# Optimization experiments

Measured on AMD Instinct MI355X. Metric: run time of the kernel, lower is better.

Reference implementation:

```python
import jax, jax.numpy as jnp
import numpy as np

B, T, D = 4, 2048, 768
D_CONV, D_GRIF, D_FFN, K = 384, 384, 2048, 3
EPS = 1e-6


def rmsnorm(x, w):
    rms = jax.lax.rsqrt(jnp.mean(jnp.square(x.astype(jnp.float32)), axis=-1, keepdims=True) + EPS)
    return (x.astype(jnp.float32) * rms).astype(x.dtype) * w


def causal_dwconv(x, w):
    # x: [B,T,C], w: [C,K] depthwise causal conv
    k = w.shape[1]
    xp = jnp.pad(x, ((0, 0), (k - 1, 0), (0, 0)))  # left pad -> causal
    out = jax.lax.conv_general_dilated(
        xp.transpose(0, 2, 1), w[:, None, :],  # [B,C,T+K-1], [C,1,K]
        window_strides=(1,), padding='VALID',
        dimension_numbers=('NCW', 'OIW', 'NCW'),
        feature_group_count=w.shape[0])
    return out.transpose(0, 2, 1)  # [B,T,C]


def rg_lru(v, r, i, lam):
    # Griffin RG-LRU: log_a = -8*softplus(lam)*r; h_t = a*h_{t-1} + sqrt(1-a^2)*(i*v)
    log_a = -8.0 * jax.nn.softplus(lam) * r                # [B,T,Dg]
    a = jnp.exp(log_a)
    gated = jnp.sqrt(jnp.maximum(1.0 - jnp.exp(2.0 * log_a), EPS)) * (i * v)
    def comb(c1, c2):
        a1, b1 = c1
        a2, b2 = c2
        return (a1 * a2, a2 * b1 + b2)
    _, h = jax.lax.associative_scan(comb, (a, gated), axis=1)
    return h


def setup_inputs() -> dict:
    key = jax.random.key(0)
    ks = jax.random.split(key, 16)
    s_in = 1.0 / np.sqrt(D)
    s_ffn = 1.0 / np.sqrt(D_FFN)
    return {
        'x': jax.random.normal(ks[0], (B, T, D), jnp.float32),
        'velocity': jnp.zeros((B, T, D), jnp.float32),
        'pre_norm_w': jnp.ones((D,), jnp.float32),
        'conv_in_w': jax.random.normal(ks[1], (D, 2 * D_CONV), jnp.float32) * s_in,
        'conv_dw_w': jax.random.normal(ks[2], (D_CONV, K), jnp.float32) * (1.0 / np.sqrt(K)),
        'grif_v_w': jax.random.normal(ks[3], (D, D_GRIF), jnp.float32) * s_in,
        'grif_r_w': jax.random.normal(ks[4], (D, D_GRIF), jnp.float32) * s_in,
        'grif_i_w': jax.random.normal(ks[5], (D, D_GRIF), jnp.float32) * s_in,
        'grif_lam': jax.random.uniform(ks[6], (D_GRIF,), jnp.float32, 0.5, 2.0),
        'out_w': jax.random.normal(ks[7], (D, D), jnp.float32) * s_in,
        'log_beta': jnp.array(0.0, jnp.float32),  # log(0.5/(1-0.5))
        'ffn_norm_w': jnp.ones((D,), jnp.float32),
        'w1': jax.random.normal(ks[8], (D, D_FFN), jnp.float32) * s_in,
        'w3': jax.random.normal(ks[9], (D, D_FFN), jnp.float32) * s_in,
        'w2': jax.random.normal(ks[10], (D_FFN, D), jnp.float32) * s_ffn,
    }


def reference(x, velocity, pre_norm_w, conv_in_w, conv_dw_w, grif_v_w, grif_r_w,
              grif_i_w, grif_lam, out_w, log_beta, ffn_norm_w, w1, w3, w2):
    xn = rmsnorm(x, pre_norm_w)
    # GatedConv branch -> [B,T,D_CONV]
    u, g = jnp.split(xn @ conv_in_w, 2, axis=-1)
    conv_out = causal_dwconv(u, conv_dw_w) * jax.nn.silu(g)
    # Griffin RG-LRU branch -> [B,T,D_GRIF]
    v = xn @ grif_v_w
    r = jax.nn.sigmoid(xn @ grif_r_w)
    i = jax.nn.sigmoid(xn @ grif_i_w)
    griffin_out = rg_lru(v, r, i, grif_lam)
    # concat -> out_proj -> momentum residual
    mixer_out = jnp.concatenate([conv_out, griffin_out], axis=-1) @ out_w
    beta = jax.nn.sigmoid(log_beta)
    velocity = beta * velocity + mixer_out
    x = x + velocity
    # ffn: RMSNorm -> SwiGLU -> residual
    normed = rmsnorm(x, ffn_norm_w)
    x = x + (jax.nn.silu(normed @ w1) * (normed @ w3)) @ w2
    return (x, velocity)
```

## Files before the change

kernel.cpp:

```cpp
#include <hip/hip_runtime.h>
#include <hip/hip_bf16.h>
#include <cstdint>

#define BSZ   4
#define TSEQ  2048
#define DMOD  768
#define DCONV 384
#define DGRIF 384
#define DFFN  2048
#define BT    (BSZ*TSEQ)
#define NG1   1920
#define EPS_  1e-6f

typedef __bf16 bf16;
typedef __bf16 bf16x8 __attribute__((ext_vector_type(8)));
typedef float  f32x4  __attribute__((ext_vector_type(4)));

__device__ __forceinline__ float sigmoidf_(float x) { return 1.f / (1.f + __expf(-x)); }

__device__ __forceinline__ void gload_lds16(const void* g, void* l) {
  __builtin_amdgcn_global_load_lds(
      (const __attribute__((address_space(1))) void*)(uintptr_t)g,
      (__attribute__((address_space(3))) void*)(uint32_t)(uintptr_t)l,
      16, 0, 0);
}

__device__ __forceinline__ int swz_wg() {
  const int nwg = gridDim.x;
  const int bid = blockIdx.x;
  const int cpx = nwg >> 3;
  return (bid & 7) * cpx + (bid >> 3);
}


template <int MODE>
__global__ __launch_bounds__(256) void transpose_bf16_kernel(
    const float* __restrict__ W, bf16* __restrict__ Wt, int R, int C, int half)
{
  __shared__ float tile[32][33];
  const int tc = blockIdx.x * 32;
  const int tr = blockIdx.y * 32;
  const int lx = threadIdx.x;
  const int ly = threadIdx.y;
  #pragma unroll
  for (int i = ly; i < 32; i += 8) {
    int r = tr + i, c = tc + lx;
    tile[i][lx] = (r < R && c < C) ? W[(size_t)r * C + c] : 0.f;
  }
  __syncthreads();
  #pragma unroll
  for (int i = ly; i < 32; i += 8) {
    int oc = tc + i;
    int orr = tr + lx;
    if (oc < C && orr < R) {
      int orow = (MODE == 0) ? oc : ((oc >> 6) << 7) + half + (oc & 63);
      Wt[(size_t)orow * R + orr] = (bf16)tile[lx][i];
    }
  }
}

__global__ __launch_bounds__(256) void rmsnorm_kernel(
    const float* __restrict__ x, const float* __restrict__ w, bf16* __restrict__ out)
{
  __shared__ float sbuf[4];
  const int row = blockIdx.x;
  const int tid = threadIdx.x;
  const float* xr = x + (size_t)row * DMOD;
  float v0 = xr[tid], v1 = xr[tid + 256], v2 = xr[tid + 512];
  float s = v0*v0 + v1*v1 + v2*v2;
  #pragma unroll
  for (int o = 32; o > 0; o >>= 1) s += __shfl_down(s, o, 64);
  if ((tid & 63) == 0) sbuf[tid >> 6] = s;
  __syncthreads();
  float tot = sbuf[0] + sbuf[1] + sbuf[2] + sbuf[3];
  float rms = rsqrtf(tot * (1.f / (float)DMOD) + EPS_);
  bf16* orow = out + (size_t)row * DMOD;
  orow[tid]       = (bf16)(v0 * rms * w[tid]);
  orow[tid + 256] = (bf16)(v1 * rms * w[tid + 256]);
  orow[tid + 512] = (bf16)(v2 * rms * w[tid + 512]);
}

__global__ __launch_bounds__(256) void gemm_w128(
    const bf16* __restrict__ A, const bf16* __restrict__ Bt, bf16* __restrict__ C,
    int M, int N, int K, int nx)
{
  __shared__ alignas(16) unsigned short As[128 * 64];
  __shared__ alignas(16) unsigned short Bs[128 * 64];

  const int wg = swz_wg();
  const int m0 = (wg / nx) * 128, n0 = (wg % nx) * 128;
  const int tid  = threadIdx.x;
  const int wave = tid >> 6;
  const int lane = tid & 63;
  const int wr = wave >> 1, wc = wave & 1;

  f32x4 acc[4][4] = {};
  const int srow = lane >> 3;
  const int scol = ((lane & 7) ^ srow) * 8;
  const int lr = lane & 15;
  const int lsw = lr & 7;
  const int lk4 = lane >> 4;

  for (int k0 = 0; k0 < K; k0 += 64) {
    __syncthreads();
    #pragma unroll
    for (int it = 0; it < 4; ++it) {
      const int chunk = wave * 4 + it;
      const int row = chunk * 8 + srow;
      gload_lds16(A  + (size_t)(m0 + row) * K + k0 + scol, (char*)As + chunk * 1024);
      gload_lds16(Bt + (size_t)(n0 + row) * K + k0 + scol, (char*)Bs + chunk * 1024);
    }
    __syncthreads();
    #pragma unroll
    for (int kk = 0; kk < 2; ++kk) {
      bf16x8 af[4], bfr[4];
      #pragma unroll
      for (int i = 0; i < 4; ++i)
        af[i] = *reinterpret_cast<const bf16x8*>(
            &As[(wr*64 + i*16 + lr) * 64 + (((kk*4 + lk4) ^ lsw) * 8)]);
      #pragma unroll
      for (int i = 0; i < 4; ++i)
        bfr[i] = *reinterpret_cast<const bf16x8*>(
            &Bs[(wc*64 + i*16 + lr) * 64 + (((kk*4 + lk4) ^ lsw) * 8)]);
      #pragma unroll
      for (int mi = 0; mi < 4; ++mi)
        #pragma unroll
        for (int ni = 0; ni < 4; ++ni)
          acc[mi][ni] = __builtin_amdgcn_mfma_f32_16x16x32_bf16(af[mi], bfr[ni], acc[mi][ni], 0, 0, 0);
    }
  }

  #pragma unroll
  for (int mi = 0; mi < 4; ++mi)
    #pragma unroll
    for (int ni = 0; ni < 4; ++ni)
      #pragma unroll
      for (int reg = 0; reg < 4; ++reg) {
        const int r = m0 + wr*64 + mi*16 + (lane >> 4) * 4 + reg;
        const int c = n0 + wc*64 + ni*16 + (lane & 15);
        C[(size_t)r * N + c] = (bf16)acc[mi][ni][reg];
      }
}

__global__ __launch_bounds__(256) void gemm_ffn13(
    const bf16* __restrict__ A, const bf16* __restrict__ Bt, bf16* __restrict__ H,
    int M, int K, int nx)
{
  __shared__ alignas(16) unsigned short As[128 * 64];
  __shared__ alignas(16) unsigned short Bs[128 * 64];
  bf16* comb = reinterpret_cast<bf16*>(As);

  const int wg = swz_wg();
  const int m0 = (wg / nx) * 128;
  const int bx = wg % nx;
  const int n0 = bx * 128;
  const int tid  = threadIdx.x;
  const int wave = tid >> 6;
  const int lane = tid & 63;
  const int wr = wave >> 1, wc = wave & 1;

  f32x4 acc[4][4] = {};
  const int srow = lane >> 3;
  const int scol = ((lane & 7) ^ srow) * 8;
  const int lr = lane & 15;
  const int lsw = lr & 7;
  const int lk4 = lane >> 4;

  for (int k0 = 0; k0 < K; k0 += 64) {
    __syncthreads();
    #pragma unroll
    for (int it = 0; it < 4; ++it) {
      const int chunk = wave * 4 + it;
      const int row = chunk * 8 + srow;
      gload_lds16(A  + (size_t)(m0 + row) * K + k0 + scol, (char*)As + chunk * 1024);
      gload_lds16(Bt + (size_t)(n0 + row) * K + k0 + scol, (char*)Bs + chunk * 1024);
    }
    __syncthreads();
    #pragma unroll
    for (int kk = 0; kk < 2; ++kk) {
      bf16x8 af[4], bfr[4];
      #pragma unroll
      for (int i = 0; i < 4; ++i)
        af[i] = *reinterpret_cast<const bf16x8*>(
            &As[(wr*64 + i*16 + lr) * 64 + (((kk*4 + lk4) ^ lsw) * 8)]);
      #pragma unroll
      for (int i = 0; i < 4; ++i)
        bfr[i] = *reinterpret_cast<const bf16x8*>(
            &Bs[(wc*64 + i*16 + lr) * 64 + (((kk*4 + lk4) ^ lsw) * 8)]);
      #pragma unroll
      for (int mi = 0; mi < 4; ++mi)
        #pragma unroll
        for (int ni = 0; ni < 4; ++ni)
          acc[mi][ni] = __builtin_amdgcn_mfma_f32_16x16x32_bf16(af[mi], bfr[ni], acc[mi][ni], 0, 0, 0);
    }
  }

  __syncthreads();
  if (wc == 1) {
    #pragma unroll
    for (int mi = 0; mi < 4; ++mi)
      #pragma unroll
      for (int ni = 0; ni < 4; ++ni)
        #pragma unroll
        for (int reg = 0; reg < 4; ++reg) {
          const int row = wr*64 + mi*16 + (lane >> 4) * 4 + reg;
          const int col = ni*16 + (lane & 15);
          comb[row * 64 + col] = (bf16)acc[mi][ni][reg];
        }
  }
  __syncthreads();
  if (wc == 0) {
    #pragma unroll
    for (int mi = 0; mi < 4; ++mi)
      #pragma unroll
      for (int ni = 0; ni < 4; ++ni)
        #pragma unroll
        for (int reg = 0; reg < 4; ++reg) {
          const int row = wr*64 + mi*16 + (lane >> 4) * 4 + reg;
          const int col = ni*16 + (lane & 15);
          float p3 = (float)comb[row * 64 + col];
          float p1 = acc[mi][ni][reg];
          H[(size_t)(m0 + row) * DFFN + bx * 64 + col] = (bf16)(p1 * sigmoidf_(p1) * p3);
        }
  }
}

template <int EPI>
__global__ __launch_bounds__(256) void gemm_n64(
    const bf16* __restrict__ A, const bf16* __restrict__ Bt, float* __restrict__ C,
    const float* __restrict__ xin, const float* __restrict__ vin,
    float* __restrict__ outv, const float* __restrict__ log_beta,
    int M, int N, int K, int nx)
{
  __shared__ alignas(16) unsigned short As[128 * 64];
  __shared__ alignas(16) unsigned short Bs[64 * 64];

  const int wg = swz_wg();
  const int m0 = (wg / nx) * 128, n0 = (wg % nx) * 64;
  const int tid  = threadIdx.x;
  const int wave = tid >> 6;
  const int lane = tid & 63;
  const int wr = wave >> 1, wc = wave & 1;

  f32x4 acc[4][2] = {};
  const int srow = lane >> 3;
  const int scol = ((lane & 7) ^ srow) * 8;
  const int lr = lane & 15;
  const int lsw = lr & 7;
  const int lk4 = lane >> 4;

  for (int k0 = 0; k0 < K; k0 += 64) {
    __syncthreads();
    #pragma unroll
    for (int it = 0; it < 6; ++it) {
      const int chunk = wave * 6 + it;
      if (chunk < 16) {
        const int row = chunk * 8 + srow;
        gload_lds16(A + (size_t)(m0 + row) * K + k0 + scol, (char*)As + chunk * 1024);
      } else {
        const int row = (chunk - 16) * 8 + srow;
        gload_lds16(Bt + (size_t)(n0 + row) * K + k0 + scol, (char*)Bs + (chunk - 16) * 1024);
      }
    }
    __syncthreads();
    #pragma unroll
    for (int kk = 0; kk < 2; ++kk) {
      bf16x8 af[4], bfr[2];
      #pragma unroll
      for (int i = 0; i < 4; ++i)
        af[i] = *reinterpret_cast<const bf16x8*>(
            &As[(wr*64 + i*16 + lr) * 64 + (((kk*4 + lk4) ^ lsw) * 8)]);
      #pragma unroll
      for (int i = 0; i < 2; ++i)
        bfr[i] = *reinterpret_cast<const bf16x8*>(
            &Bs[(wc*32 + i*16 + lr) * 64 + (((kk*4 + lk4) ^ lsw) * 8)]);
      #pragma unroll
      for (int mi = 0; mi < 4; ++mi)
        #pragma unroll
        for (int ni = 0; ni < 2; ++ni)
          acc[mi][ni] = __builtin_amdgcn_mfma_f32_16x16x32_bf16(af[mi], bfr[ni], acc[mi][ni], 0, 0, 0);
    }
  }

  const float beta = (EPI == 0) ? sigmoidf_(log_beta[0]) : 0.f;
  #pragma unroll
  for (int mi = 0; mi < 4; ++mi)
    #pragma unroll
    for (int ni = 0; ni < 2; ++ni)
      #pragma unroll
      for (int reg = 0; reg < 4; ++reg) {
        const int r = m0 + wr*64 + mi*16 + (lane >> 4) * 4 + reg;
        const int c = n0 + wc*32 + ni*16 + (lane & 15);
        const size_t off = (size_t)r * N + c;
        float v = acc[mi][ni][reg];
        if (EPI == 0) {
          float vel = beta * vin[off] + v;
          float x1  = xin[off] + vel;
          outv[off] = vel;
          C[off] = x1;
        } else {
          C[off] += v;
        }
      }
}

#define NCH  32
#define CLEN 64

__device__ __forceinline__ void lru_step(const bf16* row, int c, float coef,
                                         float& a, float& g)
{
  float v  = (float)row[2*DCONV + c];
  float r  = sigmoidf_((float)row[2*DCONV + DGRIF + c]);
  float is = sigmoidf_((float)row[2*DCONV + 2*DGRIF + c]);
  float la = coef * r;
  a = __expf(la);
  g = sqrtf(fmaxf(1.f - __expf(2.f * la), EPS_)) * (is * v);
}

__global__ __launch_bounds__(256) void lru_pass1(
    const bf16* __restrict__ g1, const float* __restrict__ lam,
    float* __restrict__ cA, float* __restrict__ cB)
{
  const int idx = blockIdx.x * 256 + threadIdx.x;
  const int c = idx % DGRIF;
  const int rest = idx / DGRIF;
  const int j = rest & (NCH - 1);
  const int b = rest / NCH;
  const float coef = -8.f * log1pf(__expf(lam[c]));
  const bf16* base = g1 + (size_t)(b * TSEQ + j * CLEN) * NG1;
  float A = 1.f, Bv = 0.f;
  #pragma unroll 4
  for (int t = 0; t < CLEN; ++t) {
    float a, g;
    lru_step(base + (size_t)t * NG1, c, coef, a, g);
    A *= a;
    Bv = a * Bv + g;
  }
  cA[((size_t)b * DGRIF + c) * NCH + j] = A;
  cB[((size_t)b * DGRIF + c) * NCH + j] = Bv;
}

__global__ __launch_bounds__(256) void lru_pass2(
    const bf16* __restrict__ g1, const float* __restrict__ lam,
    const float* __restrict__ cA, const float* __restrict__ cB,
    const float* __restrict__ dw, bf16* __restrict__ mixin)
{
  const int idx = blockIdx.x * 256 + threadIdx.x;
  const int c = idx % DGRIF;
  const int rest = idx / DGRIF;
  const int j = rest & (NCH - 1);
  const int b = rest / NCH;
  const float coef = -8.f * log1pf(__expf(lam[c]));
  float Hc = 0.f;
  const float* pa = cA + ((size_t)b * DGRIF + c) * NCH;
  const float* pb = cB + ((size_t)b * DGRIF + c) * NCH;
  for (int k = 0; k < j; ++k) Hc = pa[k] * Hc + pb[k];

  const int t0 = j * CLEN;
  const bf16* base = g1 + (size_t)(b * TSEQ + t0) * NG1;
  const float w0 = dw[c*3], w1 = dw[c*3 + 1], w2 = dw[c*3 + 2];
  float u1 = (t0 >= 1) ? (float)base[-(ptrdiff_t)NG1 + c]     : 0.f;
  float u0 = (t0 >= 2) ? (float)base[-(ptrdiff_t)(2*NG1) + c] : 0.f;

  bf16* mbase = mixin + (size_t)(b * TSEQ + t0) * DMOD;
  #pragma unroll 4
  for (int t = 0; t < CLEN; ++t) {
    const bf16* row = base + (size_t)t * NG1;
    float u2 = (float)row[c];
    float gg = (float)row[DCONV + c];
    float conv = u0 * w0 + u1 * w1 + u2 * w2;
    mbase[(size_t)t * DMOD + c] = (bf16)(conv * (gg * sigmoidf_(gg)));
    u0 = u1; u1 = u2;
    float a, g;
    lru_step(row, c, coef, a, g);
    Hc = a * Hc + g;
    mbase[(size_t)t * DMOD + DCONV + c] = (bf16)Hc;
  }
}

extern "C" void kernel_launch(void* const* d_in, const int* in_sizes, int n_in,
                              void* d_out, int out_size, void* d_ws, size_t ws_size,
                              hipStream_t stream)
{
  const float* x         = (const float*)d_in[0];
  const float* vel_in    = (const float*)d_in[1];
  const float* pre_w     = (const float*)d_in[2];
  const float* conv_in_w = (const float*)d_in[3];
  const float* conv_dw   = (const float*)d_in[4];
  const float* gv        = (const float*)d_in[5];
  const float* gr        = (const float*)d_in[6];
  const float* gi        = (const float*)d_in[7];
  const float* lam       = (const float*)d_in[8];
  const float* out_w     = (const float*)d_in[9];
  const float* log_beta  = (const float*)d_in[10];
  const float* ffn_w     = (const float*)d_in[11];
  const float* w1        = (const float*)d_in[12];
  const float* w3        = (const float*)d_in[13];
  const float* w2        = (const float*)d_in[14];

  char* ws = (char*)d_ws;
  size_t off = 0;
  auto alloc = [&](size_t bytes) { void* p = ws + off; off += (bytes + 255) & ~(size_t)255; return p; };

  bf16*  WT_G1  = (bf16*)alloc((size_t)NG1 * DMOD * 2);
  bf16*  WT_OUT = (bf16*)alloc((size_t)DMOD * DMOD * 2);
  bf16*  WT_W13 = (bf16*)alloc((size_t)2 * DFFN * DMOD * 2);
  bf16*  WT_W2  = (bf16*)alloc((size_t)DMOD * DFFN * 2);
  float* CA     = (float*)alloc((size_t)BSZ * DGRIF * NCH * 4);
  float* CB     = (float*)alloc((size_t)BSZ * DGRIF * NCH * 4);
  bf16*  XN     = (bf16*)alloc((size_t)BT * DMOD * 2);
  bf16*  G1     = (bf16*)alloc((size_t)BT * NG1 * 2);
  bf16*  MIXIN  = (bf16*)alloc((size_t)BT * DMOD * 2);
  bf16*  H      = (bf16*)alloc((size_t)BT * DFFN * 2);
  bf16*  NORMED = (bf16*)alloc((size_t)BT * DMOD * 2);

  float* OUTX   = (float*)d_out;
  float* OUTV   = OUTX + (size_t)BT * DMOD;

  const dim3 tb(32, 8);
  transpose_bf16_kernel<0><<<dim3(DMOD/32,  DMOD/32), tb, 0, stream>>>(conv_in_w, WT_G1, DMOD, DMOD, 0);
  transpose_bf16_kernel<0><<<dim3(DGRIF/32, DMOD/32), tb, 0, stream>>>(gv, WT_G1 + (size_t)(2*DCONV) * DMOD, DMOD, DGRIF, 0);
  transpose_bf16_kernel<0><<<dim3(DGRIF/32, DMOD/32), tb, 0, stream>>>(gr, WT_G1 + (size_t)(2*DCONV + DGRIF) * DMOD, DMOD, DGRIF, 0);
  transpose_bf16_kernel<0><<<dim3(DGRIF/32, DMOD/32), tb, 0, stream>>>(gi, WT_G1 + (size_t)(2*DCONV + 2*DGRIF) * DMOD, DMOD, DGRIF, 0);
  transpose_bf16_kernel<0><<<dim3(DMOD/32,  DMOD/32), tb, 0, stream>>>(out_w, WT_OUT, DMOD, DMOD, 0);
  transpose_bf16_kernel<1><<<dim3(DFFN/32,  DMOD/32), tb, 0, stream>>>(w1, WT_W13, DMOD, DFFN, 0);
  transpose_bf16_kernel<1><<<dim3(DFFN/32,  DMOD/32), tb, 0, stream>>>(w3, WT_W13, DMOD, DFFN, 64);
  transpose_bf16_kernel<0><<<dim3(DMOD/32,  DFFN/32), tb, 0, stream>>>(w2, WT_W2, DFFN, DMOD, 0);

  rmsnorm_kernel<<<BT, 256, 0, stream>>>(x, pre_w, XN);

  gemm_w128<<<(NG1/128) * (BT/128), 256, 0, stream>>>(XN, WT_G1, G1, BT, NG1, DMOD, NG1/128);

  lru_pass1<<<(BSZ * NCH * DGRIF) / 256, 256, 0, stream>>>(G1, lam, CA, CB);
  lru_pass2<<<(BSZ * NCH * DGRIF) / 256, 256, 0, stream>>>(G1, lam, CA, CB, conv_dw, MIXIN);

  gemm_n64<0><<<(DMOD/64) * (BT/128), 256, 0, stream>>>(MIXIN, WT_OUT, OUTX, x, vel_in, OUTV,
                                                        log_beta, BT, DMOD, DMOD, DMOD/64);

  rmsnorm_kernel<<<BT, 256, 0, stream>>>(OUTX, ffn_w, NORMED);

  gemm_ffn13<<<(DFFN/64) * (BT/128), 256, 0, stream>>>(NORMED, WT_W13, H, BT, DMOD, DFFN/64);

  gemm_n64<1><<<(DMOD/64) * (BT/128), 256, 0, stream>>>(H, WT_W2, OUTX, nullptr, nullptr, nullptr,
                                                        nullptr, BT, DMOD, DFFN, DMOD/64);
}
```

Measured before the change: 287.1 us.

## Replace 128x128 GEMMs with pipelined 256x256 tile kernel for G1 and FFN13

Adds a 512-thread GEMM with 256x256 tiles and double-buffered 128KB dynamic LDS. It prefetches half-K slices ahead with fine-grained vmcnt waits, and raises priority around the MFMA blocks. It replaces the G1 projection and fused W1/W3 SwiGLU GEMMs, and pads the G1 output width from 1920 to 2048 with zeroed weight rows so it divides evenly into 256-wide tiles. The aim is more data reuse per tile and load latency hidden behind MFMAs, in exchange for some wasted padded compute, heavy LDS use that may limit occupancy, and fewer workgroups per GEMM.

```diff
diff --git a/kernel.cpp b/kernel.cpp
--- a/kernel.cpp
+++ b/kernel.cpp
@@ -10,6 +10,7 @@
 #define DFFN  2048
 #define BT    (BSZ*TSEQ)
 #define NG1   1920
+#define G1LD  2048
 #define EPS_  1e-6f
 
 typedef __bf16 bf16;
@@ -32,10 +33,181 @@
   return (bid & 7) * cpx + (bid >> 3);
 }
 
+#define SBAR() __builtin_amdgcn_s_barrier()
+#define VMCNT6() asm volatile("s_waitcnt vmcnt(6)" ::: "memory")
+#define VMCNT4() asm volatile("s_waitcnt vmcnt(4)" ::: "memory")
+#define VMCNT0() asm volatile("s_waitcnt vmcnt(0)" ::: "memory")
+
+template <int EPI>
+__global__ __launch_bounds__(512, 2) void gemm256(
+    const bf16* __restrict__ A, const bf16* __restrict__ Bt, bf16* __restrict__ C,
+    int K, int nx, int ldc)
+{
+  extern __shared__ __align__(16) char lds_dyn[];
+
+  const int wg = swz_wg();
+  const int m0 = (wg / nx) * 256;
+  const int bx = wg % nx;
+  const int n0 = bx * 256;
+  const int tid  = threadIdx.x;
+  const int lane = tid & 63;
+  const int wr = (tid >> 6) >> 2;
+  const int wc = (tid >> 6) & 3;
+  const int lr = lane & 15;
+  const int lk4 = lane >> 4;
+
+  f32x4 acc[8][4] = {};
+  bf16x8 af[4], bfr[4];
+
+  const int nt = K >> 6;
+
+  auto ldA = [&](int cur, int kk, int row) -> bf16x8 {
+    const int off = (cur << 15) + (kk << 14) + row * 64 + ((lk4 ^ ((row >> 1) & 3)) << 4);
+    return *reinterpret_cast<const bf16x8*>(&lds_dyn[off]);
+  };
+  auto ldB = [&](int cur, int kk, int row) -> bf16x8 {
+    const int off = 65536 + (cur << 15) + (kk << 14) + row * 64 + ((lk4 ^ ((row >> 1) & 3)) << 4);
+    return *reinterpret_cast<const bf16x8*>(&lds_dyn[off]);
+  };
+  auto stageA = [&](int t, int kk) {
+    const bf16* g = A + (size_t)m0 * K + t * 64 + kk * 32;
+    const int dstbase = ((t & 1) << 15) + (kk << 14);
+    #pragma unroll
+    for (int p = 0; p < 2; ++p) {
+      const int f = (p << 9) + tid;
+      const int row = f >> 2;
+      const int gs = (f & 3) ^ ((row >> 1) & 3);
+      gload_lds16(g + (size_t)row * K + gs * 8,
+                  &lds_dyn[dstbase + (p << 13) + ((tid >> 6) << 10)]);
+    }
+  };
+  auto stageB = [&](int t, int kk) {
+    const bf16* g = Bt + (size_t)n0 * K + t * 64 + kk * 32;
+    const int dstbase = 65536 + ((t & 1) << 15) + (kk << 14);
+    #pragma unroll
+    for (int p = 0; p < 2; ++p) {
+      const int f = (p << 9) + tid;
+      const int row = f >> 2;
+      const int gs = (f & 3) ^ ((row >> 1) & 3);
+      gload_lds16(g + (size_t)row * K + gs * 8,
+                  &lds_dyn[dstbase + (p << 13) + ((tid >> 6) << 10)]);
+    }
+  };
+
+  stageA(0, 0); stageB(0, 0); stageA(0, 1); stageB(0, 1); stageA(1, 0);
+  VMCNT6();
+  SBAR();
+
+  for (int t = 0; t < nt; ++t) {
+    const int cur = t & 1;
+    const bool s1 = (t + 1 < nt), s2 = (t + 2 < nt);
+
+    #pragma unroll
+    for (int i = 0; i < 4; ++i) af[i] = ldA(cur, 0, wr * 128 + i * 16 + lr);
+    #pragma unroll
+    for (int i = 0; i < 4; ++i) bfr[i] = ldB(cur, 0, wc * 64 + i * 16 + lr);
+    if (s1) stageB(t + 1, 0);
+    SBAR();
+    __builtin_amdgcn_s_setprio(1);
+    #pragma unroll
+    for (int mi = 0; mi < 4; ++mi)
+      #pragma unroll
+      for (int ni = 0; ni < 4; ++ni)
+        acc[mi][ni] = __builtin_amdgcn_mfma_f32_16x16x32_bf16(af[mi], bfr[ni], acc[mi][ni], 0, 0, 0);
+    __builtin_amdgcn_s_setprio(0);
+    SBAR();
+
+    #pragma unroll
+    for (int i = 0; i < 4; ++i) af[i] = ldA(cur, 0, wr * 128 + 64 + i * 16 + lr);
+    if (s1) stageA(t + 1, 1);
+    SBAR();
+    __builtin_amdgcn_s_setprio(1);
+    #pragma unroll
+    for (int mi = 0; mi < 4; ++mi)
+      #pragma unroll
+      for (int ni = 0; ni < 4; ++ni)
+        acc[4 + mi][ni] = __builtin_amdgcn_mfma_f32_16x16x32_bf16(af[mi], bfr[ni], acc[4 + mi][ni], 0, 0, 0);
+    __builtin_amdgcn_s_setprio(0);
+    if (s1) { VMCNT6(); } else { VMCNT0(); }
+    SBAR();
+
+    #pragma unroll
+    for (int i = 0; i < 4; ++i) af[i] = ldA(cur, 1, wr * 128 + i * 16 + lr);
+    #pragma unroll
+    for (int i = 0; i < 4; ++i) bfr[i] = ldB(cur, 1, wc * 64 + i * 16 + lr);
+    if (s1) stageB(t + 1, 1);
+    SBAR();
+    __builtin_amdgcn_s_setprio(1);
+    #pragma unroll
+    for (int mi = 0; mi < 4; ++mi)
+      #pragma unroll
+      for (int ni = 0; ni < 4; ++ni)
+        acc[mi][ni] = __builtin_amdgcn_mfma_f32_16x16x32_bf16(af[mi], bfr[ni], acc[mi][ni], 0, 0, 0);
+    __builtin_amdgcn_s_setprio(0);
+    SBAR();
+
+    #pragma unroll
+    for (int i = 0; i < 4; ++i) af[i] = ldA(cur, 1, wr * 128 + 64 + i * 16 + lr);
+    if (s2) stageA(t + 2, 0);
+    SBAR();
+    __builtin_amdgcn_s_setprio(1);
+    #pragma unroll
+    for (int mi = 0; mi < 4; ++mi)
+      #pragma unroll
+      for (int ni = 0; ni < 4; ++ni)
+        acc[4 + mi][ni] = __builtin_amdgcn_mfma_f32_16x16x32_bf16(af[mi], bfr[ni], acc[4 + mi][ni], 0, 0, 0);
+    __builtin_amdgcn_s_setprio(0);
+    if (s2) { VMCNT6(); } else if (s1) { VMCNT4(); }
+    SBAR();
+  }
+
+  if (EPI == 0) {
+    #pragma unroll
+    for (int a = 0; a < 8; ++a)
+      #pragma unroll
+      for (int ni = 0; ni < 4; ++ni)
+        #pragma unroll
+        for (int reg = 0; reg < 4; ++reg) {
+          const int r = m0 + wr * 128 + a * 16 + lk4 * 4 + reg;
+          const int c = n0 + wc * 64 + ni * 16 + lr;
+          C[(size_t)r * ldc + c] = (bf16)acc[a][ni][reg];
+        }
+  } else {
+    char* comb = lds_dyn;
+    const int q = wc >> 1;
+    if (wc & 1) {
+      #pragma unroll
+      for (int a = 0; a < 8; ++a)
+        #pragma unroll
+        for (int ni = 0; ni < 4; ++ni)
+          #pragma unroll
+          for (int reg = 0; reg < 4; ++reg) {
+            const int r = wr * 128 + a * 16 + lk4 * 4 + reg;
+            const int col = ni * 16 + lr;
+            *reinterpret_cast<bf16*>(&comb[(q << 15) + r * 128 + col * 2]) = (bf16)acc[a][ni][reg];
+          }
+    }
+    SBAR();
+    if (!(wc & 1)) {
+      #pragma unroll
+      for (int a = 0; a < 8; ++a)
+        #pragma unroll
+        for (int ni = 0; ni < 4; ++ni)
+          #pragma unroll
+          for (int reg = 0; reg < 4; ++reg) {
+            const int r = wr * 128 + a * 16 + lk4 * 4 + reg;
+            const int col = ni * 16 + lr;
+            const float p3 = (float)*reinterpret_cast<const bf16*>(&comb[(q << 15) + r * 128 + col * 2]);
+            const float p1 = acc[a][ni][reg];
+            C[(size_t)(m0 + r) * ldc + (bx * 2 + q) * 64 + col] = (bf16)(p1 * sigmoidf_(p1) * p3);
+          }
+    }
+  }
+}
 
 template <int MODE>
 __global__ __launch_bounds__(256) void transpose_bf16_kernel(
-    const float* __restrict__ W, bf16* __restrict__ Wt, int R, int C, int half)
+    const float* __restrict__ W, bf16* __restrict__ Wt, int R, int C, int Cpad, int half)
 {
   __shared__ float tile[32][33];
   const int tc = blockIdx.x * 32;
@@ -52,9 +224,15 @@
   for (int i = ly; i < 32; i += 8) {
     int oc = tc + i;
     int orr = tr + lx;
-    if (oc < C && orr < R) {
-      int orow = (MODE == 0) ? oc : ((oc >> 6) << 7) + half + (oc & 63);
-      Wt[(size_t)orow * R + orr] = (bf16)tile[lx][i];
+    if (orr < R) {
+      if (MODE == 0) {
+        if (oc < Cpad) Wt[(size_t)oc * R + orr] = (bf16)tile[lx][i];
+      } else {
+        if (oc < C) {
+          int orow = ((oc >> 6) << 7) + half + (oc & 63);
+          Wt[(size_t)orow * R + orr] = (bf16)tile[lx][i];
+        }
+      }
     }
   }
 }
@@ -80,151 +258,6 @@
   orow[tid + 512] = (bf16)(v2 * rms * w[tid + 512]);
 }
 
-__global__ __launch_bounds__(256) void gemm_w128(
-    const bf16* __restrict__ A, const bf16* __restrict__ Bt, bf16* __restrict__ C,
-    int M, int N, int K, int nx)
-{
-  __shared__ alignas(16) unsigned short As[128 * 64];
-  __shared__ alignas(16) unsigned short Bs[128 * 64];
-
-  const int wg = swz_wg();
-  const int m0 = (wg / nx) * 128, n0 = (wg % nx) * 128;
-  const int tid  = threadIdx.x;
-  const int wave = tid >> 6;
-  const int lane = tid & 63;
-  const int wr = wave >> 1, wc = wave & 1;
-
-  f32x4 acc[4][4] = {};
-  const int srow = lane >> 3;
-  const int scol = ((lane & 7) ^ srow) * 8;
-  const int lr = lane & 15;
-  const int lsw = lr & 7;
-  const int lk4 = lane >> 4;
-
-  for (int k0 = 0; k0 < K; k0 += 64) {
-    __syncthreads();
-    #pragma unroll
-    for (int it = 0; it < 4; ++it) {
-      const int chunk = wave * 4 + it;
-      const int row = chunk * 8 + srow;
-      gload_lds16(A  + (size_t)(m0 + row) * K + k0 + scol, (char*)As + chunk * 1024);
-      gload_lds16(Bt + (size_t)(n0 + row) * K + k0 + scol, (char*)Bs + chunk * 1024);
-    }
-    __syncthreads();
-    #pragma unroll
-    for (int kk = 0; kk < 2; ++kk) {
-      bf16x8 af[4], bfr[4];
-      #pragma unroll
-      for (int i = 0; i < 4; ++i)
-        af[i] = *reinterpret_cast<const bf16x8*>(
-            &As[(wr*64 + i*16 + lr) * 64 + (((kk*4 + lk4) ^ lsw) * 8)]);
-      #pragma unroll
-      for (int i = 0; i < 4; ++i)
-        bfr[i] = *reinterpret_cast<const bf16x8*>(
-            &Bs[(wc*64 + i*16 + lr) * 64 + (((kk*4 + lk4) ^ lsw) * 8)]);
-      #pragma unroll
-      for (int mi = 0; mi < 4; ++mi)
-        #pragma unroll
-        for (int ni = 0; ni < 4; ++ni)
-          acc[mi][ni] = __builtin_amdgcn_mfma_f32_16x16x32_bf16(af[mi], bfr[ni], acc[mi][ni], 0, 0, 0);
-    }
-  }
-
-  #pragma unroll
-  for (int mi = 0; mi < 4; ++mi)
-    #pragma unroll
-    for (int ni = 0; ni < 4; ++ni)
-      #pragma unroll
-      for (int reg = 0; reg < 4; ++reg) {
-        const int r = m0 + wr*64 + mi*16 + (lane >> 4) * 4 + reg;
-        const int c = n0 + wc*64 + ni*16 + (lane & 15);
-        C[(size_t)r * N + c] = (bf16)acc[mi][ni][reg];
-      }
-}
-
-__global__ __launch_bounds__(256) void gemm_ffn13(
-    const bf16* __restrict__ A, const bf16* __restrict__ Bt, bf16* __restrict__ H,
-    int M, int K, int nx)
-{
-  __shared__ alignas(16) unsigned short As[128 * 64];
-  __shared__ alignas(16) unsigned short Bs[128 * 64];
-  bf16* comb = reinterpret_cast<bf16*>(As);
-
-  const int wg = swz_wg();
-  const int m0 = (wg / nx) * 128;
-  const int bx = wg % nx;
-  const int n0 = bx * 128;
-  const int tid  = threadIdx.x;
-  const int wave = tid >> 6;
-  const int lane = tid & 63;
-  const int wr = wave >> 1, wc = wave & 1;
-
-  f32x4 acc[4][4] = {};
-  const int srow = lane >> 3;
-  const int scol = ((lane & 7) ^ srow) * 8;
-  const int lr = lane & 15;
-  const int lsw = lr & 7;
-  const int lk4 = lane >> 4;
-
-  for (int k0 = 0; k0 < K; k0 += 64) {
-    __syncthreads();
-    #pragma unroll
-    for (int it = 0; it < 4; ++it) {
-      const int chunk = wave * 4 + it;
-      const int row = chunk * 8 + srow;
-      gload_lds16(A  + (size_t)(m0 + row) * K + k0 + scol, (char*)As + chunk * 1024);
-      gload_lds16(Bt + (size_t)(n0 + row) * K + k0 + scol, (char*)Bs + chunk * 1024);
-    }
-    __syncthreads();
-    #pragma unroll
-    for (int kk = 0; kk < 2; ++kk) {
-      bf16x8 af[4], bfr[4];
-      #pragma unroll
-      for (int i = 0; i < 4; ++i)
-        af[i] = *reinterpret_cast<const bf16x8*>(
-            &As[(wr*64 + i*16 + lr) * 64 + (((kk*4 + lk4) ^ lsw) * 8)]);
-      #pragma unroll
-      for (int i = 0; i < 4; ++i)
-        bfr[i] = *reinterpret_cast<const bf16x8*>(
-            &Bs[(wc*64 + i*16 + lr) * 64 + (((kk*4 + lk4) ^ lsw) * 8)]);
-      #pragma unroll
-      for (int mi = 0; mi < 4; ++mi)
-        #pragma unroll
-        for (int ni = 0; ni < 4; ++ni)
-          acc[mi][ni] = __builtin_amdgcn_mfma_f32_16x16x32_bf16(af[mi], bfr[ni], acc[mi][ni], 0, 0, 0);
-    }
-  }
-
-  __syncthreads();
-  if (wc == 1) {
-    #pragma unroll
-    for (int mi = 0; mi < 4; ++mi)
-      #pragma unroll
-      for (int ni = 0; ni < 4; ++ni)
-        #pragma unroll
-        for (int reg = 0; reg < 4; ++reg) {
-          const int row = wr*64 + mi*16 + (lane >> 4) * 4 + reg;
-          const int col = ni*16 + (lane & 15);
-          comb[row * 64 + col] = (bf16)acc[mi][ni][reg];
-        }
-  }
-  __syncthreads();
-  if (wc == 0) {
-    #pragma unroll
-    for (int mi = 0; mi < 4; ++mi)
-      #pragma unroll
-      for (int ni = 0; ni < 4; ++ni)
-        #pragma unroll
-        for (int reg = 0; reg < 4; ++reg) {
-          const int row = wr*64 + mi*16 + (lane >> 4) * 4 + reg;
-          const int col = ni*16 + (lane & 15);
-          float p3 = (float)comb[row * 64 + col];
-          float p1 = acc[mi][ni][reg];
-          H[(size_t)(m0 + row) * DFFN + bx * 64 + col] = (bf16)(p1 * sigmoidf_(p1) * p3);
-        }
-  }
-}
-
 template <int EPI>
 __global__ __launch_bounds__(256) void gemm_n64(
     const bf16* __restrict__ A, const bf16* __restrict__ Bt, float* __restrict__ C,
@@ -328,12 +361,12 @@
   const int j = rest & (NCH - 1);
   const int b = rest / NCH;
   const float coef = -8.f * log1pf(__expf(lam[c]));
-  const bf16* base = g1 + (size_t)(b * TSEQ + j * CLEN) * NG1;
+  const bf16* base = g1 + (size_t)(b * TSEQ + j * CLEN) * G1LD;
   float A = 1.f, Bv = 0.f;
   #pragma unroll 4
   for (int t = 0; t < CLEN; ++t) {
     float a, g;
-    lru_step(base + (size_t)t * NG1, c, coef, a, g);
+    lru_step(base + (size_t)t * G1LD, c, coef, a, g);
     A *= a;
     Bv = a * Bv + g;
   }
@@ -358,15 +391,15 @@
   for (int k = 0; k < j; ++k) Hc = pa[k] * Hc + pb[k];
 
   const int t0 = j * CLEN;
-  const bf16* base = g1 + (size_t)(b * TSEQ + t0) * NG1;
+  const bf16* base = g1 + (size_t)(b * TSEQ + t0) * G1LD;
   const float w0 = dw[c*3], w1 = dw[c*3 + 1], w2 = dw[c*3 + 2];
-  float u1 = (t0 >= 1) ? (float)base[-(ptrdiff_t)NG1 + c]     : 0.f;
-  float u0 = (t0 >= 2) ? (float)base[-(ptrdiff_t)(2*NG1) + c] : 0.f;
+  float u1 = (t0 >= 1) ? (float)base[-(ptrdiff_t)G1LD + c]     : 0.f;
+  float u0 = (t0 >= 2) ? (float)base[-(ptrdiff_t)(2*G1LD) + c] : 0.f;
 
   bf16* mbase = mixin + (size_t)(b * TSEQ + t0) * DMOD;
   #pragma unroll 4
   for (int t = 0; t < CLEN; ++t) {
-    const bf16* row = base + (size_t)t * NG1;
+    const bf16* row = base + (size_t)t * G1LD;
     float u2 = (float)row[c];
     float gg = (float)row[DCONV + c];
     float conv = u0 * w0 + u1 * w1 + u2 * w2;
@@ -403,14 +436,14 @@
   size_t off = 0;
   auto alloc = [&](size_t bytes) { void* p = ws + off; off += (bytes + 255) & ~(size_t)255; return p; };
 
-  bf16*  WT_G1  = (bf16*)alloc((size_t)NG1 * DMOD * 2);
+  bf16*  WT_G1  = (bf16*)alloc((size_t)G1LD * DMOD * 2);
   bf16*  WT_OUT = (bf16*)alloc((size_t)DMOD * DMOD * 2);
   bf16*  WT_W13 = (bf16*)alloc((size_t)2 * DFFN * DMOD * 2);
   bf16*  WT_W2  = (bf16*)alloc((size_t)DMOD * DFFN * 2);
   float* CA     = (float*)alloc((size_t)BSZ * DGRIF * NCH * 4);
   float* CB     = (float*)alloc((size_t)BSZ * DGRIF * NCH * 4);
   bf16*  XN     = (bf16*)alloc((size_t)BT * DMOD * 2);
-  bf16*  G1     = (bf16*)alloc((size_t)BT * NG1 * 2);
+  bf16*  G1     = (bf16*)alloc((size_t)BT * G1LD * 2);
   bf16*  MIXIN  = (bf16*)alloc((size_t)BT * DMOD * 2);
   bf16*  H      = (bf16*)alloc((size_t)BT * DFFN * 2);
   bf16*  NORMED = (bf16*)alloc((size_t)BT * DMOD * 2);
@@ -418,19 +451,23 @@
   float* OUTX   = (float*)d_out;
   float* OUTV   = OUTX + (size_t)BT * DMOD;
 
+  hipFuncSetAttribute((const void*)gemm256<0>, hipFuncAttributeMaxDynamicSharedMemorySize, 131072);
+  hipFuncSetAttribute((const void*)gemm256<1>, hipFuncAttributeMaxDynamicSharedMemorySize, 131072);
+
   const dim3 tb(32, 8);
-  transpose_bf16_kernel<0><<<dim3(DMOD/32,  DMOD/32), tb, 0, stream>>>(conv_in_w, WT_G1, DMOD, DMOD, 0);
-  transpose_bf16_kernel<0><<<dim3(DGRIF/32, DMOD/32), tb, 0, stream>>>(gv, WT_G1 + (size_t)(2*DCONV) * DMOD, DMOD, DGRIF, 0);
-  transpose_bf16_kernel<0><<<dim3(DGRIF/32, DMOD/32), tb, 0, stream>>>(gr, WT_G1 + (size_t)(2*DCONV + DGRIF) * DMOD, DMOD, DGRIF, 0);
-  transpose_bf16_kernel<0><<<dim3(DGRIF/32, DMOD/32), tb, 0, stream>>>(gi, WT_G1 + (size_t)(2*DCONV + 2*DGRIF) * DMOD, DMOD, DGRIF, 0);
-  transpose_bf16_kernel<0><<<dim3(DMOD/32,  DMOD/32), tb, 0, stream>>>(out_w, WT_OUT, DMOD, DMOD, 0);
-  transpose_bf16_kernel<1><<<dim3(DFFN/32,  DMOD/32), tb, 0, stream>>>(w1, WT_W13, DMOD, DFFN, 0);
-  transpose_bf16_kernel<1><<<dim3(DFFN/32,  DMOD/32), tb, 0, stream>>>(w3, WT_W13, DMOD, DFFN, 64);
-  transpose_bf16_kernel<0><<<dim3(DMOD/32,  DFFN/32), tb, 0, stream>>>(w2, WT_W2, DFFN, DMOD, 0);
+  hipMemsetAsync(WT_G1 + (size_t)NG1 * DMOD, 0, (size_t)(G1LD - NG1) * DMOD * 2, stream);
+  transpose_bf16_kernel<0><<<dim3(DMOD/32,  DMOD/32), tb, 0, stream>>>(conv_in_w, WT_G1, DMOD, DMOD, DMOD, 0);
+  transpose_bf16_kernel<0><<<dim3(DGRIF/32, DMOD/32), tb, 0, stream>>>(gv, WT_G1 + (size_t)(2*DCONV) * DMOD, DMOD, DGRIF, DGRIF, 0);
+  transpose_bf16_kernel<0><<<dim3(DGRIF/32, DMOD/32), tb, 0, stream>>>(gr, WT_G1 + (size_t)(2*DCONV + DGRIF) * DMOD, DMOD, DGRIF, DGRIF, 0);
+  transpose_bf16_kernel<0><<<dim3(DGRIF/32, DMOD/32), tb, 0, stream>>>(gi, WT_G1 + (size_t)(2*DCONV + 2*DGRIF) * DMOD, DMOD, DGRIF, DGRIF, 0);
+  transpose_bf16_kernel<0><<<dim3(DMOD/32,  DMOD/32), tb, 0, stream>>>(out_w, WT_OUT, DMOD, DMOD, DMOD, 0);
+  transpose_bf16_kernel<1><<<dim3(DFFN/32,  DMOD/32), tb, 0, stream>>>(w1, WT_W13, DMOD, DFFN, DFFN, 0);
+  transpose_bf16_kernel<1><<<dim3(DFFN/32,  DMOD/32), tb, 0, stream>>>(w3, WT_W13, DMOD, DFFN, DFFN, 64);
+  transpose_bf16_kernel<0><<<dim3(DMOD/32,  DFFN/32), tb, 0, stream>>>(w2, WT_W2, DFFN, DMOD, DMOD, 0);
 
   rmsnorm_kernel<<<BT, 256, 0, stream>>>(x, pre_w, XN);
 
-  gemm_w128<<<(NG1/128) * (BT/128), 256, 0, stream>>>(XN, WT_G1, G1, BT, NG1, DMOD, NG1/128);
+  gemm256<0><<<(BT/256) * (G1LD/256), 512, 131072, stream>>>(XN, WT_G1, G1, DMOD, G1LD/256, G1LD);
 
   lru_pass1<<<(BSZ * NCH * DGRIF) / 256, 256, 0, stream>>>(G1, lam, CA, CB);
   lru_pass2<<<(BSZ * NCH * DGRIF) / 256, 256, 0, stream>>>(G1, lam, CA, CB, conv_dw, MIXIN);
@@ -440,7 +477,7 @@
 
   rmsnorm_kernel<<<BT, 256, 0, stream>>>(OUTX, ffn_w, NORMED);
 
-  gemm_ffn13<<<(DFFN/64) * (BT/128), 256, 0, stream>>>(NORMED, WT_W13, H, BT, DMOD, DFFN/64);
+  gemm256<1><<<(BT/256) * (2*DFFN/256), 512, 131072, stream>>>(NORMED, WT_W13, H, DMOD, 2*DFFN/256, DFFN);
 
   gemm_n64<1><<<(DMOD/64) * (BT/128), 256, 0, stream>>>(H, WT_W2, OUTX, nullptr, nullptr, nullptr,
                                                         nullptr, BT, DMOD, DFFN, DMOD/64);
```

Measured after the change: 290.9 us. No clear change (+1.3%).

## Merge weight transposes into one launch and enlarge FFN13 GEMM tile to 256 rows

Applied to the files above, without the earlier changes.

Replaces the eight per-weight transpose launches with a single kernel that maps each block index to a weight matrix and tile. Changes the fused w1/w3 GEMM to 512-thread blocks covering 256 rows, so each loaded B tile is reused across twice as many A rows, and updates the swizzled LDS load and read indexing to match. The aim is to cut launch overhead and B-tile global traffic, at the cost of more LDS per block and possibly fewer resident blocks per CU.

```diff
diff --git a/kernel.cpp b/kernel.cpp
--- a/kernel.cpp
+++ b/kernel.cpp
@@ -32,16 +32,30 @@
   return (bid & 7) * cpx + (bid >> 3);
 }
 
-
-template <int MODE>
-__global__ __launch_bounds__(256) void transpose_bf16_kernel(
-    const float* __restrict__ W, bf16* __restrict__ Wt, int R, int C, int half)
+__global__ __launch_bounds__(256) void transpose_all(
+    const float* __restrict__ conv_in_w, const float* __restrict__ gv,
+    const float* __restrict__ gr, const float* __restrict__ gi,
+    const float* __restrict__ out_w, const float* __restrict__ w1,
+    const float* __restrict__ w3, const float* __restrict__ w2,
+    bf16* __restrict__ WT_G1, bf16* __restrict__ WT_OUT,
+    bf16* __restrict__ WT_W13, bf16* __restrict__ WT_W2)
 {
   __shared__ float tile[32][33];
-  const int tc = blockIdx.x * 32;
-  const int tr = blockIdx.y * 32;
-  const int lx = threadIdx.x;
-  const int ly = threadIdx.y;
+  int t = blockIdx.x;
+  const float* W; bf16* Wt; int R, C, mode = 0, half = 0;
+  if      (t < 576)  {           W = conv_in_w; Wt = WT_G1;                        R = 768;  C = 768; }
+  else if (t < 864)  { t -= 576;  W = gv;  Wt = WT_G1 + (size_t)768  * DMOD;       R = 768;  C = 384; }
+  else if (t < 1152) { t -= 864;  W = gr;  Wt = WT_G1 + (size_t)1152 * DMOD;       R = 768;  C = 384; }
+  else if (t < 1440) { t -= 1152; W = gi;  Wt = WT_G1 + (size_t)1536 * DMOD;       R = 768;  C = 384; }
+  else if (t < 2016) { t -= 1440; W = out_w; Wt = WT_OUT;                          R = 768;  C = 768; }
+  else if (t < 3552) { t -= 2016; W = w1;  Wt = WT_W13; mode = 1; half = 0;        R = 768;  C = 2048; }
+  else if (t < 5088) { t -= 3552; W = w3;  Wt = WT_W13; mode = 1; half = 64;       R = 768;  C = 2048; }
+  else               { t -= 5088; W = w2;  Wt = WT_W2;                             R = 2048; C = 768; }
+
+  const int xt = C >> 5;
+  const int tc = (t % xt) * 32, tr = (t / xt) * 32;
+  const int lx = threadIdx.x & 31;
+  const int ly = threadIdx.x >> 5;
   #pragma unroll
   for (int i = ly; i < 32; i += 8) {
     int r = tr + i, c = tc + lx;
@@ -53,7 +67,7 @@
     int oc = tc + i;
     int orr = tr + lx;
     if (oc < C && orr < R) {
-      int orow = (MODE == 0) ? oc : ((oc >> 6) << 7) + half + (oc & 63);
+      int orow = (mode == 0) ? oc : ((oc >> 6) << 7) + half + (oc & 63);
       Wt[(size_t)orow * R + orr] = (bf16)tile[lx][i];
     }
   }
@@ -136,57 +150,66 @@
     for (int ni = 0; ni < 4; ++ni)
       #pragma unroll
       for (int reg = 0; reg < 4; ++reg) {
-        const int r = m0 + wr*64 + mi*16 + (lane >> 4) * 4 + reg;
-        const int c = n0 + wc*64 + ni*16 + (lane & 15);
+        const int r = m0 + wr*64 + mi*16 + lk4 * 4 + reg;
+        const int c = n0 + wc*64 + ni*16 + lr;
         C[(size_t)r * N + c] = (bf16)acc[mi][ni][reg];
       }
 }
 
-__global__ __launch_bounds__(256) void gemm_ffn13(
+__global__ __launch_bounds__(512) void gemm_ffn13b(
     const bf16* __restrict__ A, const bf16* __restrict__ Bt, bf16* __restrict__ H,
     int M, int K, int nx)
 {
-  __shared__ alignas(16) unsigned short As[128 * 64];
+  __shared__ alignas(16) unsigned short As[256 * 64];
   __shared__ alignas(16) unsigned short Bs[128 * 64];
   bf16* comb = reinterpret_cast<bf16*>(As);
 
   const int wg = swz_wg();
-  const int m0 = (wg / nx) * 128;
+  const int m0 = (wg / nx) * 256;
   const int bx = wg % nx;
   const int n0 = bx * 128;
   const int tid  = threadIdx.x;
   const int wave = tid >> 6;
   const int lane = tid & 63;
-  const int wr = wave >> 1, wc = wave & 1;
+  const int wr = wave >> 1;
+  const int wc = wave & 1;
+  const int lr = lane & 15;
+  const int lk4 = lane >> 4;
 
   f32x4 acc[4][4] = {};
-  const int srow = lane >> 3;
-  const int scol = ((lane & 7) ^ srow) * 8;
-  const int lr = lane & 15;
-  const int lsw = lr & 7;
-  const int lk4 = lane >> 4;
 
   for (int k0 = 0; k0 < K; k0 += 64) {
     __syncthreads();
     #pragma unroll
-    for (int it = 0; it < 4; ++it) {
-      const int chunk = wave * 4 + it;
-      const int row = chunk * 8 + srow;
-      gload_lds16(A  + (size_t)(m0 + row) * K + k0 + scol, (char*)As + chunk * 1024);
-      gload_lds16(Bt + (size_t)(n0 + row) * K + k0 + scol, (char*)Bs + chunk * 1024);
+    for (int p = 0; p < 4; ++p) {
+      const int f = (p << 9) + tid;
+      const int row = f >> 3;
+      const int gs = (f & 7) ^ (row & 7);
+      gload_lds16(A + (size_t)(m0 + row) * K + k0 + gs * 8,
+                  (char*)As + (p << 13) + (wave << 10));
+    }
+    #pragma unroll
+    for (int p = 0; p < 2; ++p) {
+      const int f = (p << 9) + tid;
+      const int row = f >> 3;
+      const int gs = (f & 7) ^ (row & 7);
+      gload_lds16(Bt + (size_t)(n0 + row) * K + k0 + gs * 8,
+                  (char*)Bs + (p << 13) + (wave << 10));
     }
     __syncthreads();
     #pragma unroll
     for (int kk = 0; kk < 2; ++kk) {
       bf16x8 af[4], bfr[4];
       #pragma unroll
-      for (int i = 0; i < 4; ++i)
-        af[i] = *reinterpret_cast<const bf16x8*>(
-            &As[(wr*64 + i*16 + lr) * 64 + (((kk*4 + lk4) ^ lsw) * 8)]);
-      #pragma unroll
-      for (int i = 0; i < 4; ++i)
-        bfr[i] = *reinterpret_cast<const bf16x8*>(
-            &Bs[(wc*64 + i*16 + lr) * 64 + (((kk*4 + lk4) ^ lsw) * 8)]);
+      for (int i = 0; i < 4; ++i) {
+        const int r = wr*64 + i*16 + lr;
+        af[i] = *reinterpret_cast<const bf16x8*>(&As[r * 64 + (((kk*4 + lk4) ^ (r & 7)) * 8)]);
+      }
+      #pragma unroll
+      for (int i = 0; i < 4; ++i) {
+        const int r = wc*64 + i*16 + lr;
+        bfr[i] = *reinterpret_cast<const bf16x8*>(&Bs[r * 64 + (((kk*4 + lk4) ^ (r & 7)) * 8)]);
+      }
       #pragma unroll
       for (int mi = 0; mi < 4; ++mi)
         #pragma unroll
@@ -203,8 +226,8 @@
       for (int ni = 0; ni < 4; ++ni)
         #pragma unroll
         for (int reg = 0; reg < 4; ++reg) {
-          const int row = wr*64 + mi*16 + (lane >> 4) * 4 + reg;
-          const int col = ni*16 + (lane & 15);
+          const int row = wr*64 + mi*16 + lk4 * 4 + reg;
+          const int col = ni*16 + lr;
           comb[row * 64 + col] = (bf16)acc[mi][ni][reg];
         }
   }
@@ -216,8 +239,8 @@
       for (int ni = 0; ni < 4; ++ni)
         #pragma unroll
         for (int reg = 0; reg < 4; ++reg) {
-          const int row = wr*64 + mi*16 + (lane >> 4) * 4 + reg;
-          const int col = ni*16 + (lane & 15);
+          const int row = wr*64 + mi*16 + lk4 * 4 + reg;
+          const int col = ni*16 + lr;
           float p3 = (float)comb[row * 64 + col];
           float p1 = acc[mi][ni][reg];
           H[(size_t)(m0 + row) * DFFN + bx * 64 + col] = (bf16)(p1 * sigmoidf_(p1) * p3);
@@ -289,8 +312,8 @@
     for (int ni = 0; ni < 2; ++ni)
       #pragma unroll
       for (int reg = 0; reg < 4; ++reg) {
-        const int r = m0 + wr*64 + mi*16 + (lane >> 4) * 4 + reg;
-        const int c = n0 + wc*32 + ni*16 + (lane & 15);
+        const int r = m0 + wr*64 + mi*16 + lk4 * 4 + reg;
+        const int c = n0 + wc*32 + ni*16 + lr;
         const size_t off = (size_t)r * N + c;
         float v = acc[mi][ni][reg];
         if (EPI == 0) {
@@ -418,15 +441,8 @@
   float* OUTX   = (float*)d_out;
   float* OUTV   = OUTX + (size_t)BT * DMOD;
 
-  const dim3 tb(32, 8);
-  transpose_bf16_kernel<0><<<dim3(DMOD/32,  DMOD/32), tb, 0, stream>>>(conv_in_w, WT_G1, DMOD, DMOD, 0);
-  transpose_bf16_kernel<0><<<dim3(DGRIF/32, DMOD/32), tb, 0, stream>>>(gv, WT_G1 + (size_t)(2*DCONV) * DMOD, DMOD, DGRIF, 0);
-  transpose_bf16_kernel<0><<<dim3(DGRIF/32, DMOD/32), tb, 0, stream>>>(gr, WT_G1 + (size_t)(2*DCONV + DGRIF) * DMOD, DMOD, DGRIF, 0);
-  transpose_bf16_kernel<0><<<dim3(DGRIF/32, DMOD/32), tb, 0, stream>>>(gi, WT_G1 + (size_t)(2*DCONV + 2*DGRIF) * DMOD, DMOD, DGRIF, 0);
-  transpose_bf16_kernel<0><<<dim3(DMOD/32,  DMOD/32), tb, 0, stream>>>(out_w, WT_OUT, DMOD, DMOD, 0);
-  transpose_bf16_kernel<1><<<dim3(DFFN/32,  DMOD/32), tb, 0, stream>>>(w1, WT_W13, DMOD, DFFN, 0);
-  transpose_bf16_kernel<1><<<dim3(DFFN/32,  DMOD/32), tb, 0, stream>>>(w3, WT_W13, DMOD, DFFN, 64);
-  transpose_bf16_kernel<0><<<dim3(DMOD/32,  DFFN/32), tb, 0, stream>>>(w2, WT_W2, DFFN, DMOD, 0);
+  transpose_all<<<6624, 256, 0, stream>>>(conv_in_w, gv, gr, gi, out_w, w1, w3, w2,
+                                          WT_G1, WT_OUT, WT_W13, WT_W2);
 
   rmsnorm_kernel<<<BT, 256, 0, stream>>>(x, pre_w, XN);
 
@@ -440,7 +456,7 @@
 
   rmsnorm_kernel<<<BT, 256, 0, stream>>>(OUTX, ffn_w, NORMED);
 
-  gemm_ffn13<<<(DFFN/64) * (BT/128), 256, 0, stream>>>(NORMED, WT_W13, H, BT, DMOD, DFFN/64);
+  gemm_ffn13b<<<(BT/256) * (DFFN/64), 512, 0, stream>>>(NORMED, WT_W13, H, BT, DMOD, DFFN/64);
 
   gemm_n64<1><<<(DMOD/64) * (BT/128), 256, 0, stream>>>(H, WT_W2, OUTX, nullptr, nullptr, nullptr,
                                                         nullptr, BT, DMOD, DFFN, DMOD/64);
```

Measured after the change: 263.5 us. 8.2% less time.
